# Optimization experiments

Measured on AMD Instinct MI355X. Metric: run time of the kernel, lower is better.

## Reference

```python
import jax, jax.numpy as jnp
import numpy as np

N_SRC = 50000
N_DST = 50000
E = 500000
H = 128
ED = 32
EPS = 1e-5


def _linear_params(key, fan_in, fan_out):
    kw, kb = jax.random.split(key)
    bound = 1.0 / np.sqrt(fan_in)
    W = jax.random.uniform(kw, (fan_in, fan_out), jnp.float32, -bound, bound)
    b = jax.random.uniform(kb, (fan_out,), jnp.float32, -bound, bound)
    return W, b


def setup_inputs() -> dict:
    key = jax.random.key(0)
    ks = jax.random.split(key, 12)
    src_x = jax.random.normal(ks[0], (N_SRC, H), jnp.float32)
    dst_x = jax.random.normal(ks[1], (N_DST, H), jnp.float32)
    edge_index = jax.random.randint(ks[2], (2, E), 0, N_DST, jnp.int64)
    edge_attr = jax.random.normal(ks[3], (E, ED), jnp.float32)
    Wsrc, bsrc = _linear_params(ks[4], H, H)
    Wdst, bdst = _linear_params(ks[5], H, H)
    We, be = _linear_params(ks[6], ED, H)
    Wattn, battn = _linear_params(ks[7], 3 * H, 1)
    Wmsg, bmsg = _linear_params(ks[8], H, H)
    Wout, bout = _linear_params(ks[9], 2 * H, H)
    gamma = jnp.ones((H,), jnp.float32)
    beta = jnp.zeros((H,), jnp.float32)
    return dict(src_x=src_x, dst_x=dst_x, edge_index=edge_index, edge_attr=edge_attr,
                Wsrc=Wsrc, bsrc=bsrc, Wdst=Wdst, bdst=bdst, We=We, be=be,
                Wattn=Wattn, battn=battn, Wmsg=Wmsg, bmsg=bmsg,
                Wout=Wout, bout=bout, gamma=gamma, beta=beta)


def _segment_softmax(scores, idx, num_segments):
    # numerically stable softmax over variable-size segments of dst index
    m = jax.ops.segment_max(scores, idx, num_segments=num_segments)
    ex = jnp.exp(scores - m[idx])
    s = jax.ops.segment_sum(ex, idx, num_segments=num_segments)
    return ex / s[idx]


def reference(src_x, dst_x, edge_index, edge_attr,
              Wsrc, bsrc, Wdst, bdst, We, be,
              Wattn, battn, Wmsg, bmsg, Wout, bout, gamma, beta):
    src_idx = edge_index[0]
    dst_idx = edge_index[1]
    num_dst = dst_x.shape[0]

    src_feat = src_x[src_idx] @ Wsrc + bsrc          # [E, H]
    dst_feat = dst_x[dst_idx] @ Wdst + bdst          # [E, H]
    e_feat = edge_attr @ We + be                     # [E, H]

    attn_in = jnp.concatenate([src_feat, dst_feat, e_feat], axis=-1)  # [E, 3H]
    msg = (src_feat + e_feat) @ Wmsg + bmsg          # [E, H]

    scores = (jnp.tanh(attn_in) @ Wattn + battn)[:, 0]  # [E]
    alpha = _segment_softmax(scores, dst_idx, num_dst)   # [E]

    agg = jax.ops.segment_sum(msg * alpha[:, None], dst_idx, num_segments=num_dst)  # [num_dst, H]

    updated = jnp.concatenate([dst_x, agg], axis=-1) @ Wout + bout
    # dropout is identity in eval mode
    h = dst_x + updated
    mu = jnp.mean(h, axis=-1, keepdims=True)
    var = jnp.var(h, axis=-1, keepdims=True)
    return (h - mu) * jax.lax.rsqrt(var + EPS) * gamma + beta
```

## Files before the change

kernel.cpp:

```cpp
#include <hip/hip_runtime.h>
#include <math.h>

#define NSRC 50000
#define NDST 50000
#define NE   500000
#define HD   128
#define EDIM 32
#define LN_EPS 1e-5f

typedef __attribute__((ext_vector_type(8))) short short8;
typedef __attribute__((ext_vector_type(4))) float f32x4;
typedef unsigned short u16;

#define TL2E 2.8853900817779268f
#define L2E  1.4426950408889634f

__device__ __forceinline__ float EXP2(float x) {
#if __has_builtin(__builtin_amdgcn_exp2f)
    return __builtin_amdgcn_exp2f(x);
#else
    return exp2f(x);
#endif
}
__device__ __forceinline__ float RCP(float x) {
#if __has_builtin(__builtin_amdgcn_rcpf)
    return __builtin_amdgcn_rcpf(x);
#else
    return 1.f / x;
#endif
}
__device__ __forceinline__ u16 f2b(float x) {
    unsigned u = __float_as_uint(x);
    return (u16)((u + 0x7FFFu + ((u >> 16) & 1u)) >> 16);
}
__device__ __forceinline__ float b2f(u16 h) {
    return __uint_as_float(((unsigned)h) << 16);
}
__device__ __forceinline__ short8 ld8(const u16* p) { return *(const short8*)p; }

__global__ __launch_bounds__(128) void fold1_kernel(
    const float* __restrict__ Wsrc, const float* __restrict__ bsrc,
    const float* __restrict__ We,   const float* __restrict__ be,
    const float* __restrict__ Wmsg, const float* __restrict__ bmsg,
    float* __restrict__ Wsm, float* __restrict__ bsm,
    float* __restrict__ WeMsg, float* __restrict__ c2,
    int* __restrict__ cnt)
{
    const int j = threadIdx.x;
    const int r = blockIdx.x;
    if (r >= 162) {
        int i = (r - 162) * 128 + j;
        if (i < NDST + 16) cnt[i] = 0;
        return;
    }
    float s = 0.f;
    if (r < 128) {
        for (int k = 0; k < 128; ++k) s += Wsrc[r*HD + k] * Wmsg[k*HD + j];
        Wsm[r*HD + j] = s;
    } else if (r < 160) {
        const int rr = r - 128;
        for (int k = 0; k < 128; ++k) s += We[rr*HD + k] * Wmsg[k*HD + j];
        WeMsg[rr*HD + j] = s;
    } else if (r == 160) {
        for (int k = 0; k < 128; ++k) s += bsrc[k] * Wmsg[k*HD + j];
        bsm[j] = s + bmsg[j];
    } else {
        for (int k = 0; k < 128; ++k) s += be[k] * Wmsg[k*HD + j];
        c2[j] = s;
    }
}

__global__ __launch_bounds__(64) void pack_all_kernel(
    const float* __restrict__ Wsrc, const float* __restrict__ Wdst,
    const float* __restrict__ Wsm,  const float* __restrict__ Wout,
    const float* __restrict__ We,   const float* __restrict__ WeMsg,
    const float* __restrict__ c2,   const float* __restrict__ bout,
    u16* __restrict__ Wsrc_pk, u16* __restrict__ Wdst_pk,
    u16* __restrict__ Wsm_pk,  u16* __restrict__ W1_pk,
    u16* __restrict__ W2_pk,   u16* __restrict__ We_pk,
    u16* __restrict__ W3_pk,   float* __restrict__ bias2)
{
    const int b = blockIdx.x;
    const int lane = threadIdx.x;
    const int ln = lane & 15, quad = lane >> 4;
    const float* Wout2 = Wout + HD*HD;

    if (b == 176) {
#pragma unroll
        for (int h = 0; h < 2; ++h) {
            const int col = lane + h*64;
            float s = 0.f;
            for (int k = 0; k < 128; ++k) s += c2[k] * Wout2[k*HD + col];
            bias2[col] = bout[col] + s;
        }
        return;
    }
    if (b >= 168) {
        const int t = b - 168;
        const int jj = t*16 + ln;
        float sacc[8] = {0,0,0,0,0,0,0,0};
        for (int k = 0; k < 128; ++k) {
            const float w2 = Wout2[k*HD + jj];
#pragma unroll
            for (int j = 0; j < 8; ++j)
                sacc[j] = fmaf(WeMsg[(quad*8 + j)*HD + k], w2, sacc[j]);
        }
        u16 tmp[8];
#pragma unroll
        for (int j = 0; j < 8; ++j) tmp[j] = f2b(sacc[j]);
        *(short8*)(W3_pk + (size_t)(t*64 + lane)*8) = *(short8*)tmp;
        return;
    }

    const float* src; u16* dst; int lb; float scl = 1.f; bool addI = false;
    if      (b < 32)  { src = Wsrc; dst = Wsrc_pk; lb = b;       scl = TL2E; }
    else if (b < 64)  { src = Wdst; dst = Wdst_pk; lb = b - 32;  scl = TL2E; }
    else if (b < 96)  { src = Wsm;  dst = Wsm_pk;  lb = b - 64; }
    else if (b < 128) { src = Wout; dst = W1_pk;   lb = b - 96;  addI = true; }
    else if (b < 160) { src = Wout2;dst = W2_pk;   lb = b - 128; }
    else              { src = We;   dst = We_pk;   lb = b - 160; scl = TL2E; }
    const int kc = lb >> 3, t = lb & 7;
    u16 tmp[8];
#pragma unroll
    for (int j = 0; j < 8; ++j) {
        const int i = kc*32 + quad*8 + j, jj = t*16 + ln;
        float v = src[(size_t)i*HD + jj] * scl;
        if (addI && i == jj) v += 1.f;
        tmp[j] = f2b(v);
    }
    *(short8*)(dst + (size_t)(lb*64 + lane)*8) = *(short8*)tmp;
}

#define GN 782
#define HB ((NE + 255) / 256)

__global__ __launch_bounds__(256) void mega_kernel(
    const float* __restrict__ src_x, const float* __restrict__ dst_x,
    const int* __restrict__ ei,
    const u16* __restrict__ Wsrc_pk, const u16* __restrict__ Wsm_pk,
    const u16* __restrict__ Wdst_pk,
    const float* __restrict__ bsrc, const float* __restrict__ bsm,
    const float* __restrict__ bdst, const float* __restrict__ wattn,
    float* __restrict__ s1, float* __restrict__ s2,
    u16* __restrict__ srcmsgb, int* __restrict__ cnt, int* __restrict__ rank)
{
    __shared__ u16 lds[4 * 16 * HD];
    const int t = threadIdx.x;
    const int blk = blockIdx.x;

    if (blk >= 2*GN) {
        const int e = (blk - 2*GN) * 256 + t;
        if (e < NE) rank[e] = atomicAdd(&cnt[ei[NE + e]], 1);
        return;
    }

    const int w = t >> 6, lane = t & 63;
    const int ln = lane & 15, quad = lane >> 4;
    const bool is_src = (blk < GN);
    const int b = is_src ? blk : blk - GN;
    int row0 = (b * 4 + w) * 16;
    if (row0 > NSRC - 16) row0 = NSRC - 16;

    const float* xp = (is_src ? src_x : dst_x) + (size_t)(row0 + ln)*HD;
    short8 a[4];
#pragma unroll
    for (int kc = 0; kc < 4; ++kc) {
        float4 f0 = *(const float4*)(xp + kc*32 + quad*8);
        float4 f1 = *(const float4*)(xp + kc*32 + quad*8 + 4);
        u16 tb[8] = { f2b(f0.x), f2b(f0.y), f2b(f0.z), f2b(f0.w),
                      f2b(f1.x), f2b(f1.y), f2b(f1.z), f2b(f1.w) };
        a[kc] = *(short8*)tb;
    }

    const u16*   Wpk = is_src ? Wsrc_pk : Wdst_pk;
    const float* bb_ = is_src ? bsrc : bdst;
    const float* wa  = is_src ? wattn : wattn + HD;
    float* sout      = is_src ? s1 : s2;

    float v[4] = {0.f, 0.f, 0.f, 0.f};
    float ws = 0.f;
#pragma unroll
    for (int tt = 0; tt < 8; ++tt) {
        const float bb = bb_[tt*16 + ln] * TL2E;
        const float ww = wa[tt*16 + ln];
        f32x4 acc = {bb, bb, bb, bb};
#pragma unroll
        for (int kc = 0; kc < 4; ++kc) {
            short8 bfr = ld8(Wpk + (size_t)((kc*8 + tt)*64 + lane)*8);
            acc = __builtin_amdgcn_mfma_f32_16x16x32_bf16(a[kc], bfr, acc, 0, 0, 0);
        }
        ws += ww;
#pragma unroll
        for (int r = 0; r < 4; ++r)
            v[r] = fmaf(ww, RCP(EXP2(acc[r]) + 1.f), v[r]);
    }
#pragma unroll
    for (int off = 8; off >= 1; off >>= 1) {
        ws += __shfl_xor(ws, off);
#pragma unroll
        for (int r = 0; r < 4; ++r) v[r] += __shfl_xor(v[r], off);
    }
    if (ln == 0) {
#pragma unroll
        for (int r = 0; r < 4; ++r)
            sout[row0 + quad*4 + r] = fmaf(-2.f, v[r], ws);
    }

    if (!is_src) return;

#pragma unroll
    for (int tt = 0; tt < 8; ++tt) {
        const float bs = bsm[tt*16 + ln];
        f32x4 acc = {bs, bs, bs, bs};
#pragma unroll
        for (int kc = 0; kc < 4; ++kc) {
            short8 bfr = ld8(Wsm_pk + (size_t)((kc*8 + tt)*64 + lane)*8);
            acc = __builtin_amdgcn_mfma_f32_16x16x32_bf16(a[kc], bfr, acc, 0, 0, 0);
        }
#pragma unroll
        for (int r = 0; r < 4; ++r)
            lds[w*2048 + (quad*4 + r)*HD + tt*16 + ln] = f2b(acc[r]);
    }
    __syncthreads();
#pragma unroll
    for (int r = 0; r < 4; ++r) {
        int idx = r*512 + lane*8;
        short8 val = *(short8*)(lds + w*2048 + idx);
        int row = idx >> 7, col = idx & 127;
        *(short8*)(srcmsgb + (size_t)(row0 + row)*HD + col) = val;
    }
}

__global__ __launch_bounds__(1024) void scan1_kernel(
    const int* __restrict__ cnt, int* __restrict__ excl, int* __restrict__ bsum)
{
    __shared__ int buf[1024];
    const int t = threadIdx.x;
    const int i = blockIdx.x * 1024 + t;
    int v = (i < NDST) ? cnt[i] : 0;
    buf[t] = v;
    __syncthreads();
    for (int off = 1; off < 1024; off <<= 1) {
        int tv = (t >= off) ? buf[t - off] : 0;
        __syncthreads();
        buf[t] += tv;
        __syncthreads();
    }
    if (i < NDST) excl[i] = buf[t] - v;
    if (t == 1023) bsum[blockIdx.x] = buf[1023];
}

__global__ __launch_bounds__(256) void scan23_kernel(
    const int* __restrict__ bsum, int* __restrict__ rowptr)
{
    __shared__ int pref[64];
    const int t = threadIdx.x;
    const int NB = (NDST + 1023) / 1024;
    if (t < 64) {
        int orig = (t < NB) ? bsum[t] : 0;
        int v = orig;
        for (int off = 1; off < 64; off <<= 1) {
            int u = __shfl_up(v, off);
            if (t >= off) v += u;
        }
        pref[t] = v - orig;
        if (blockIdx.x == 0 && t == NB - 1) rowptr[NDST] = v;
    }
    __syncthreads();
    const int i = blockIdx.x * 256 + t;
    if (i < NDST) rowptr[i] += pref[i >> 10];
}

__global__ __launch_bounds__(256) void edge_score_kernel(
    const int* __restrict__ ei, const float* __restrict__ eattr,
    const u16* __restrict__ We_pk, const float* __restrict__ be,
    const float* __restrict__ wattn, const float* __restrict__ battn,
    const float* __restrict__ s1, const float* __restrict__ s2,
    const int* __restrict__ rowptr, const int* __restrict__ rank,
    int4* __restrict__ ev16)
{
    const int t = threadIdx.x;
    const int w = t >> 6, lane = t & 63;
    const int ln = lane & 15, quad = lane >> 4;
    const int e0 = (blockIdx.x * 4 + w) * 16;
    if (e0 >= NE) return;

    const float* ap = eattr + (size_t)(e0 + ln)*EDIM + quad*8;
    float4 f0 = *(const float4*)(ap);
    float4 f1 = *(const float4*)(ap + 4);
    u16 ab[8] = { f2b(f0.x), f2b(f0.y), f2b(f0.z), f2b(f0.w),
                  f2b(f1.x), f2b(f1.y), f2b(f1.z), f2b(f1.w) };
    short8 a = *(short8*)ab;

    const float* wa3 = wattn + 2*HD;
    float v[4] = {0.f, 0.f, 0.f, 0.f};
    float ws = 0.f;
#pragma unroll
    for (int tt = 0; tt < 8; ++tt) {
        const float bb = be[tt*16 + ln] * TL2E;
        const float ww = wa3[tt*16 + ln];
        f32x4 acc = {bb, bb, bb, bb};
        short8 b = ld8(We_pk + (size_t)(tt*64 + lane)*8);
        acc = __builtin_amdgcn_mfma_f32_16x16x32_bf16(a, b, acc, 0, 0, 0);
        ws += ww;
#pragma unroll
        for (int r = 0; r < 4; ++r)
            v[r] = fmaf(ww, RCP(EXP2(acc[r]) + 1.f), v[r]);
    }
#pragma unroll
    for (int off = 8; off >= 1; off >>= 1) {
        ws += __shfl_xor(ws, off);
#pragma unroll
        for (int r = 0; r < 4; ++r) v[r] += __shfl_xor(v[r], off);
    }
    const int srcq = (ln >> 2) << 4;
    float sv0 = __shfl(v[0], srcq);
    float sv1 = __shfl(v[1], srcq);
    float sv2 = __shfl(v[2], srcq);
    float sv3 = __shfl(v[3], srcq);
    const int rr = ln & 3;
    float vlo = (rr & 1) ? sv1 : sv0;
    float vhi = (rr & 1) ? sv3 : sv2;
    float vv  = (rr & 2) ? vhi : vlo;

    if (quad == 0) {
        const int e = e0 + ln;
        const int srcn = ei[e];
        const int dstn = ei[NE + e];
        float sc = (fmaf(-2.f, vv, ws) + s1[srcn] + s2[dstn] + battn[0]) * L2E;
        const int pos = rowptr[dstn] + rank[e];
        ev16[pos] = make_int4(srcn, e, __float_as_int(sc), 0);
    }
}

__global__ __launch_bounds__(256) void dst_agg_kernel(
    const int4* __restrict__ ev16, const int* __restrict__ rowptr,
    const u16* __restrict__ srcmsgb, const float* __restrict__ eattr,
    const float* __restrict__ c2,
    u16* __restrict__ aggSb, u16* __restrict__ weab)
{
    const int lane = threadIdx.x & 63;
    const int d = blockIdx.x * 4 + (threadIdx.x >> 6);
    const int el = lane >> 4, c = lane & 15;
    const int start = rowptr[d], end = rowptr[d + 1];

    if (start == end) {
        if (el == 0) {
            u16 z[8];
#pragma unroll
            for (int j = 0; j < 8; ++j) z[j] = f2b(-c2[c*8 + j]);
            *(short8*)(aggSb + (size_t)d*HD + c*8) = *(short8*)z;
            if (c < 8) {
                u16 zz[4] = {0,0,0,0};
                *(ushort4*)(weab + (size_t)d*EDIM + c*4) = *(ushort4*)zz;
            }
        }
        return;
    }

    float sacc = 0.f;
    float acc[8]  = {0,0,0,0,0,0,0,0};
    float wacc[4] = {0,0,0,0};

    int icur = start + el;
    bool vcur = (icur < end);
    int iicur = vcur ? icur : start;
    int4 q = ev16[iicur];

    for (int i0 = start; i0 < end; i0 += 4) {
        const float wgt = vcur ? EXP2(__int_as_float(q.z)) : 0.f;
        const int   srow = q.x;
        const int   ecur = q.y;
        const int inx = i0 + 4 + el;
        vcur = (inx < end);
        iicur = vcur ? inx : start;
        q = ev16[iicur];

        sacc += wgt;
        short8 sm = ld8(srcmsgb + (size_t)srow*HD + c*8);
#pragma unroll
        for (int j = 0; j < 8; ++j)
            acc[j] = fmaf(wgt, b2f(((u16*)&sm)[j]), acc[j]);
        if (c < 8) {
            float4 f = *(const float4*)(eattr + (size_t)ecur*EDIM + c*4);
            wacc[0] = fmaf(wgt, f.x, wacc[0]);
            wacc[1] = fmaf(wgt, f.y, wacc[1]);
            wacc[2] = fmaf(wgt, f.z, wacc[2]);
            wacc[3] = fmaf(wgt, f.w, wacc[3]);
        }
    }
#pragma unroll
    for (int off = 16; off <= 32; off <<= 1) {
        sacc += __shfl_xor(sacc, off);
#pragma unroll
        for (int j = 0; j < 8; ++j) acc[j] += __shfl_xor(acc[j], off);
#pragma unroll
        for (int j = 0; j < 4; ++j) wacc[j] += __shfl_xor(wacc[j], off);
    }
    const float inv = RCP(sacc);
    if (el == 0) {
        u16 o[8];
#pragma unroll
        for (int j = 0; j < 8; ++j) o[j] = f2b(acc[j] * inv);
        *(short8*)(aggSb + (size_t)d*HD + c*8) = *(short8*)o;
        if (c < 8) {
            u16 o2[4];
#pragma unroll
            for (int j = 0; j < 4; ++j) o2[j] = f2b(wacc[j] * inv);
            *(ushort4*)(weab + (size_t)d*EDIM + c*4) = *(ushort4*)o2;
        }
    }
}

__global__ __launch_bounds__(256) void final_kernel(
    const float* __restrict__ dst_x, const u16* __restrict__ aggSb,
    const u16* __restrict__ weab,
    const u16* __restrict__ W1_pk, const u16* __restrict__ W2_pk,
    const u16* __restrict__ W3_pk, const float* __restrict__ bias2,
    const float* __restrict__ gamma, const float* __restrict__ beta,
    float* __restrict__ out)
{
    const int t = threadIdx.x;
    const int w = t >> 6, lane = t & 63;
    const int ln = lane & 15, quad = lane >> 4;
    int row0 = (blockIdx.x * 4 + w) * 16;
    if (row0 > NDST - 16) row0 = NDST - 16;

    const float* rp = dst_x + (size_t)(row0 + ln)*HD;
    short8 a1[4], a2[4], a3;
#pragma unroll
    for (int kc = 0; kc < 4; ++kc) {
        float4 f0 = *(const float4*)(rp + kc*32 + quad*8);
        float4 f1 = *(const float4*)(rp + kc*32 + quad*8 + 4);
        u16 tb[8] = { f2b(f0.x), f2b(f0.y), f2b(f0.z), f2b(f0.w),
                      f2b(f1.x), f2b(f1.y), f2b(f1.z), f2b(f1.w) };
        a1[kc] = *(short8*)tb;
        a2[kc] = ld8(aggSb + (size_t)(row0 + ln)*HD + kc*32 + quad*8);
    }
    a3 = ld8(weab + (size_t)(row0 + ln)*EDIM + quad*8);

    f32x4 accs[8];
#pragma unroll
    for (int tt = 0; tt < 8; ++tt) {
        const float bb = bias2[tt*16 + ln];
        f32x4 acc = {bb, bb, bb, bb};
#pragma unroll
        for (int kc = 0; kc < 4; ++kc) {
            short8 b = ld8(W1_pk + (size_t)((kc*8 + tt)*64 + lane)*8);
            acc = __builtin_amdgcn_mfma_f32_16x16x32_bf16(a1[kc], b, acc, 0, 0, 0);
        }
#pragma unroll
        for (int kc = 0; kc < 4; ++kc) {
            short8 b = ld8(W2_pk + (size_t)((kc*8 + tt)*64 + lane)*8);
            acc = __builtin_amdgcn_mfma_f32_16x16x32_bf16(a2[kc], b, acc, 0, 0, 0);
        }
        {
            short8 b = ld8(W3_pk + (size_t)(tt*64 + lane)*8);
            acc = __builtin_amdgcn_mfma_f32_16x16x32_bf16(a3, b, acc, 0, 0, 0);
        }
        accs[tt] = acc;
    }

    const float gl[8] = { gamma[ln], gamma[16+ln], gamma[32+ln], gamma[48+ln],
                          gamma[64+ln], gamma[80+ln], gamma[96+ln], gamma[112+ln] };
    const float bl[8] = { beta[ln], beta[16+ln], beta[32+ln], beta[48+ln],
                          beta[64+ln], beta[80+ln], beta[96+ln], beta[112+ln] };
#pragma unroll
    for (int r = 0; r < 4; ++r) {
        float s = 0.f, qq = 0.f;
#pragma unroll
        for (int tt = 0; tt < 8; ++tt) {
            float u = accs[tt][r];
            s += u; qq += u*u;
        }
#pragma unroll
        for (int off = 8; off >= 1; off >>= 1) {
            s  += __shfl_xor(s, off);
            qq += __shfl_xor(qq, off);
        }
        const float mean = s * (1.f / HD);
        const float var  = qq * (1.f / HD) - mean * mean;
        const float rstd = rsqrtf(var + LN_EPS);
        const int row = row0 + quad*4 + r;
#pragma unroll
        for (int tt = 0; tt < 8; ++tt)
            out[(size_t)row*HD + tt*16 + ln] =
                (accs[tt][r] - mean) * rstd * gl[tt] + bl[tt];
    }
}

extern "C" void kernel_launch(void* const* d_in, const int* in_sizes, int n_in,
                              void* d_out, int out_size, void* d_ws, size_t ws_size,
                              hipStream_t stream)
{
    const float* src_x = (const float*)d_in[0];
    const float* dst_x = (const float*)d_in[1];
    const int*   ei    = (const int*)d_in[2];
    const float* eattr = (const float*)d_in[3];
    const float* Wsrc  = (const float*)d_in[4];
    const float* bsrc  = (const float*)d_in[5];
    const float* Wdst  = (const float*)d_in[6];
    const float* bdst  = (const float*)d_in[7];
    const float* We    = (const float*)d_in[8];
    const float* be    = (const float*)d_in[9];
    const float* Wattn = (const float*)d_in[10];
    const float* battn = (const float*)d_in[11];
    const float* Wmsg  = (const float*)d_in[12];
    const float* bmsg  = (const float*)d_in[13];
    const float* Wout  = (const float*)d_in[14];
    const float* bout  = (const float*)d_in[15];
    const float* gamma = (const float*)d_in[16];
    const float* beta  = (const float*)d_in[17];
    float* out = (float*)d_out;

    float* ws = (float*)d_ws;
    u16* srcmsgb = (u16*)(ws + 0);
    u16* aggSb   = (u16*)(ws + 3200000);
    u16* weab    = (u16*)(ws + 6400000);
    float* s1    = ws + 7200000;
    float* s2    = ws + 7250048;
    float* Wsm   = ws + 7300096;
    float* bsm   = ws + 7316480;
    float* WeMsg = ws + 7316608;
    float* c2    = ws + 7320704;
    float* bias2 = ws + 7320832;
    u16* Wsrc_pk = (u16*)(ws + 7320960);
    u16* Wdst_pk = (u16*)(ws + 7329152);
    u16* Wsm_pk  = (u16*)(ws + 7337344);
    u16* W1_pk   = (u16*)(ws + 7345536);
    u16* W2_pk   = (u16*)(ws + 7353728);
    u16* We_pk   = (u16*)(ws + 7361920);
    u16* W3_pk   = (u16*)(ws + 7363968);
    int* rowptr  = (int*)(ws + 7366016);
    int* cnt     = (int*)(ws + 7416032);
    int* bsum    = (int*)(ws + 7466048);
    int* rank    = (int*)(ws + 7466112);
    int4* ev16   = (int4*)(ws + 7966112);

    fold1_kernel<<<553, 128, 0, stream>>>(Wsrc, bsrc, We, be, Wmsg, bmsg,
                                          Wsm, bsm, WeMsg, c2, cnt);
    pack_all_kernel<<<177, 64, 0, stream>>>(Wsrc, Wdst, Wsm, Wout, We, WeMsg,
                                            c2, bout,
                                            Wsrc_pk, Wdst_pk, Wsm_pk, W1_pk,
                                            W2_pk, We_pk, W3_pk, bias2);

    mega_kernel<<<2*GN + HB, 256, 0, stream>>>(
        src_x, dst_x, ei, Wsrc_pk, Wsm_pk, Wdst_pk,
        bsrc, bsm, bdst, Wattn, s1, s2, srcmsgb, cnt, rank);

    scan1_kernel<<<(NDST + 1023) / 1024, 1024, 0, stream>>>(cnt, rowptr, bsum);
    scan23_kernel<<<(NDST + 255) / 256, 256, 0, stream>>>(bsum, rowptr);

    edge_score_kernel<<<(NE/16 + 3) / 4, 256, 0, stream>>>(
        ei, eattr, We_pk, be, Wattn, battn, s1, s2, rowptr, rank, ev16);

    dst_agg_kernel<<<NDST / 4, 256, 0, stream>>>(ev16, rowptr, srcmsgb,
                                                 eattr, c2, aggSb, weab);

    final_kernel<<<GN, 256, 0, stream>>>(dst_x, aggSb, weab, W1_pk, W2_pk, W3_pk,
                                         bias2, gamma, beta, out);
}
```

Measured before the change: 305.8 us.

## Merge weight prep kernels, stage weights in LDS, process 32 rows per wave

Merges the fold and pack preprocessing kernels into one prep kernel that computes Wsrc·Wmsg, We·Wmsg and the folded biases directly in packed bf16 form, removing a launch and the intermediate fp32 buffers. In mega_kernel each wave now handles two 16-row tiles that share B fragments staged once per block in LDS, and the message tile store uses an XOR-swizzled LDS layout. The edge-count atomics are vectorized to four edges per thread. The cost is more LDS and registers per block and extra redundant FMA work in the small prep blocks.

```diff
diff --git a/kernel.cpp b/kernel.cpp
--- a/kernel.cpp
+++ b/kernel.cpp
@@ -38,92 +38,112 @@
 }
 __device__ __forceinline__ short8 ld8(const u16* p) { return *(const short8*)p; }
 
-__global__ __launch_bounds__(128) void fold1_kernel(
+__global__ __launch_bounds__(64) void prep_kernel(
     const float* __restrict__ Wsrc, const float* __restrict__ bsrc,
-    const float* __restrict__ We,   const float* __restrict__ be,
-    const float* __restrict__ Wmsg, const float* __restrict__ bmsg,
-    float* __restrict__ Wsm, float* __restrict__ bsm,
-    float* __restrict__ WeMsg, float* __restrict__ c2,
-    int* __restrict__ cnt)
-{
-    const int j = threadIdx.x;
-    const int r = blockIdx.x;
-    if (r >= 162) {
-        int i = (r - 162) * 128 + j;
-        if (i < NDST + 16) cnt[i] = 0;
-        return;
-    }
-    float s = 0.f;
-    if (r < 128) {
-        for (int k = 0; k < 128; ++k) s += Wsrc[r*HD + k] * Wmsg[k*HD + j];
-        Wsm[r*HD + j] = s;
-    } else if (r < 160) {
-        const int rr = r - 128;
-        for (int k = 0; k < 128; ++k) s += We[rr*HD + k] * Wmsg[k*HD + j];
-        WeMsg[rr*HD + j] = s;
-    } else if (r == 160) {
-        for (int k = 0; k < 128; ++k) s += bsrc[k] * Wmsg[k*HD + j];
-        bsm[j] = s + bmsg[j];
-    } else {
-        for (int k = 0; k < 128; ++k) s += be[k] * Wmsg[k*HD + j];
-        c2[j] = s;
-    }
-}
-
-__global__ __launch_bounds__(64) void pack_all_kernel(
-    const float* __restrict__ Wsrc, const float* __restrict__ Wdst,
-    const float* __restrict__ Wsm,  const float* __restrict__ Wout,
-    const float* __restrict__ We,   const float* __restrict__ WeMsg,
-    const float* __restrict__ c2,   const float* __restrict__ bout,
+    const float* __restrict__ Wdst, const float* __restrict__ We,
+    const float* __restrict__ be,   const float* __restrict__ Wmsg,
+    const float* __restrict__ bmsg, const float* __restrict__ Wout,
+    const float* __restrict__ bout,
     u16* __restrict__ Wsrc_pk, u16* __restrict__ Wdst_pk,
-    u16* __restrict__ Wsm_pk,  u16* __restrict__ W1_pk,
-    u16* __restrict__ W2_pk,   u16* __restrict__ We_pk,
-    u16* __restrict__ W3_pk,   float* __restrict__ bias2)
-{
+    u16* __restrict__ W1_pk,   u16* __restrict__ W2_pk,
+    u16* __restrict__ We_pk,   u16* __restrict__ Wsm_pk,
+    u16* __restrict__ W3_pk,
+    float* __restrict__ bsm, float* __restrict__ c2g,
+    float* __restrict__ bias2, int* __restrict__ cnt)
+{
+    __shared__ float sbuf[32 * 128];
     const int b = blockIdx.x;
     const int lane = threadIdx.x;
+
+    if (b >= 178) {
+        const int i4 = (b - 178) * 64 + lane;
+        if (i4 < 12504) ((int4*)cnt)[i4] = make_int4(0, 0, 0, 0);
+        return;
+    }
+
     const int ln = lane & 15, quad = lane >> 4;
     const float* Wout2 = Wout + HD*HD;
 
+    if (b == 177) {
+#pragma unroll
+        for (int h = 0; h < 2; ++h) {
+            const int col = lane + h*64;
+            float s = bmsg[col];
+            for (int m = 0; m < 128; ++m) s = fmaf(bsrc[m], Wmsg[m*HD + col], s);
+            bsm[col] = s;
+        }
+        return;
+    }
     if (b == 176) {
 #pragma unroll
         for (int h = 0; h < 2; ++h) {
             const int col = lane + h*64;
             float s = 0.f;
-            for (int k = 0; k < 128; ++k) s += c2[k] * Wout2[k*HD + col];
-            bias2[col] = bout[col] + s;
+            for (int m = 0; m < 128; ++m) s = fmaf(be[m], Wmsg[m*HD + col], s);
+            sbuf[col] = s;
+            c2g[col] = s;
+        }
+        __syncthreads();
+#pragma unroll
+        for (int h = 0; h < 2; ++h) {
+            const int col = lane + h*64;
+            float s = bout[col];
+            for (int k = 0; k < 128; ++k) s = fmaf(sbuf[k], Wout2[k*HD + col], s);
+            bias2[col] = s;
         }
         return;
     }
     if (b >= 168) {
-        const int t = b - 168;
-        const int jj = t*16 + ln;
-        float sacc[8] = {0,0,0,0,0,0,0,0};
+        const int tq = b - 168;
+        const int i = lane >> 1, k0 = (lane & 1) * 64;
+        for (int k = k0; k < k0 + 64; ++k) {
+            float s = 0.f;
+            for (int m = 0; m < 128; ++m) s = fmaf(We[i*HD + m], Wmsg[m*HD + k], s);
+            sbuf[i*128 + k] = s;
+        }
+        __syncthreads();
+        const int jj = tq*16 + ln;
+        float s[8] = {0,0,0,0,0,0,0,0};
         for (int k = 0; k < 128; ++k) {
             const float w2 = Wout2[k*HD + jj];
 #pragma unroll
             for (int j = 0; j < 8; ++j)
-                sacc[j] = fmaf(WeMsg[(quad*8 + j)*HD + k], w2, sacc[j]);
+                s[j] = fmaf(sbuf[(quad*8 + j)*128 + k], w2, s[j]);
         }
         u16 tmp[8];
 #pragma unroll
-        for (int j = 0; j < 8; ++j) tmp[j] = f2b(sacc[j]);
-        *(short8*)(W3_pk + (size_t)(t*64 + lane)*8) = *(short8*)tmp;
+        for (int j = 0; j < 8; ++j) tmp[j] = f2b(s[j]);
+        *(short8*)(W3_pk + (size_t)(tq*64 + lane)*8) = *(short8*)tmp;
         return;
     }
+    if (b >= 136) {
+        const int lb = b - 136, kc = lb >> 3, tq = lb & 7;
+        const int jj = tq*16 + ln;
+        float s[8] = {0,0,0,0,0,0,0,0};
+        for (int k = 0; k < 128; ++k) {
+            const float wm = Wmsg[k*HD + jj];
+#pragma unroll
+            for (int j = 0; j < 8; ++j)
+                s[j] = fmaf(Wsrc[(size_t)(kc*32 + quad*8 + j)*HD + k], wm, s[j]);
+        }
+        u16 tmp[8];
+#pragma unroll
+        for (int j = 0; j < 8; ++j) tmp[j] = f2b(s[j]);
+        *(short8*)(Wsm_pk + (size_t)(lb*64 + lane)*8) = *(short8*)tmp;
+        return;
+    }
 
     const float* src; u16* dst; int lb; float scl = 1.f; bool addI = false;
-    if      (b < 32)  { src = Wsrc; dst = Wsrc_pk; lb = b;       scl = TL2E; }
-    else if (b < 64)  { src = Wdst; dst = Wdst_pk; lb = b - 32;  scl = TL2E; }
-    else if (b < 96)  { src = Wsm;  dst = Wsm_pk;  lb = b - 64; }
-    else if (b < 128) { src = Wout; dst = W1_pk;   lb = b - 96;  addI = true; }
-    else if (b < 160) { src = Wout2;dst = W2_pk;   lb = b - 128; }
-    else              { src = We;   dst = We_pk;   lb = b - 160; scl = TL2E; }
-    const int kc = lb >> 3, t = lb & 7;
+    if      (b < 32)  { src = Wsrc;  dst = Wsrc_pk; lb = b;       scl = TL2E; }
+    else if (b < 64)  { src = Wdst;  dst = Wdst_pk; lb = b - 32;  scl = TL2E; }
+    else if (b < 96)  { src = Wout;  dst = W1_pk;   lb = b - 64;  addI = true; }
+    else if (b < 128) { src = Wout2; dst = W2_pk;   lb = b - 96; }
+    else              { src = We;    dst = We_pk;   lb = b - 128; scl = TL2E; }
+    const int kc = lb >> 3, tq = lb & 7;
     u16 tmp[8];
 #pragma unroll
     for (int j = 0; j < 8; ++j) {
-        const int i = kc*32 + quad*8 + j, jj = t*16 + ln;
+        const int i = kc*32 + quad*8 + j, jj = tq*16 + ln;
         float v = src[(size_t)i*HD + jj] * scl;
         if (addI && i == jj) v += 1.f;
         tmp[j] = f2b(v);
@@ -131,8 +151,8 @@
     *(short8*)(dst + (size_t)(lb*64 + lane)*8) = *(short8*)tmp;
 }
 
-#define GN 782
-#define HB ((NE + 255) / 256)
+#define NBLK 391
+#define HB4 ((NE/4 + 255) / 256)
 
 __global__ __launch_bounds__(256) void mega_kernel(
     const float* __restrict__ src_x, const float* __restrict__ dst_x,
@@ -144,90 +164,135 @@
     float* __restrict__ s1, float* __restrict__ s2,
     u16* __restrict__ srcmsgb, int* __restrict__ cnt, int* __restrict__ rank)
 {
-    __shared__ u16 lds[4 * 16 * HD];
+    __shared__ __align__(16) u16 wlds[16384];
+    __shared__ __align__(16) u16 tlds[4][2048];
     const int t = threadIdx.x;
     const int blk = blockIdx.x;
 
-    if (blk >= 2*GN) {
-        const int e = (blk - 2*GN) * 256 + t;
-        if (e < NE) rank[e] = atomicAdd(&cnt[ei[NE + e]], 1);
+    if (blk >= 2*NBLK) {
+        const int idx = (blk - 2*NBLK) * 256 + t;
+        if (idx < NE/4) {
+            int4 d4 = ((const int4*)(ei + NE))[idx];
+            int4 r4;
+            r4.x = atomicAdd(&cnt[d4.x], 1);
+            r4.y = atomicAdd(&cnt[d4.y], 1);
+            r4.z = atomicAdd(&cnt[d4.z], 1);
+            r4.w = atomicAdd(&cnt[d4.w], 1);
+            ((int4*)rank)[idx] = r4;
+        }
         return;
     }
 
     const int w = t >> 6, lane = t & 63;
     const int ln = lane & 15, quad = lane >> 4;
-    const bool is_src = (blk < GN);
-    const int b = is_src ? blk : blk - GN;
-    int row0 = (b * 4 + w) * 16;
-    if (row0 > NSRC - 16) row0 = NSRC - 16;
-
-    const float* xp = (is_src ? src_x : dst_x) + (size_t)(row0 + ln)*HD;
-    short8 a[4];
+    const bool is_src = (blk < NBLK);
+    const int b = is_src ? blk : blk - NBLK;
+    int row0 = b * 128 + w * 32;
+    if (row0 > NSRC - 32) row0 = NSRC - 32;
+
+    const float* X = is_src ? src_x : dst_x;
+    const float* rp0 = X + (size_t)(row0 + ln)*HD;
+    const float* rp1 = rp0 + (size_t)16*HD;
+    short8 a0[4], a1[4];
 #pragma unroll
     for (int kc = 0; kc < 4; ++kc) {
-        float4 f0 = *(const float4*)(xp + kc*32 + quad*8);
-        float4 f1 = *(const float4*)(xp + kc*32 + quad*8 + 4);
+        float4 f0 = *(const float4*)(rp0 + kc*32 + quad*8);
+        float4 f1 = *(const float4*)(rp0 + kc*32 + quad*8 + 4);
+        float4 g0 = *(const float4*)(rp1 + kc*32 + quad*8);
+        float4 g1 = *(const float4*)(rp1 + kc*32 + quad*8 + 4);
         u16 tb[8] = { f2b(f0.x), f2b(f0.y), f2b(f0.z), f2b(f0.w),
                       f2b(f1.x), f2b(f1.y), f2b(f1.z), f2b(f1.w) };
-        a[kc] = *(short8*)tb;
-    }
-
-    const u16*   Wpk = is_src ? Wsrc_pk : Wdst_pk;
+        a0[kc] = *(short8*)tb;
+        u16 tc[8] = { f2b(g0.x), f2b(g0.y), f2b(g0.z), f2b(g0.w),
+                      f2b(g1.x), f2b(g1.y), f2b(g1.z), f2b(g1.w) };
+        a1[kc] = *(short8*)tc;
+    }
+
+    const u16* Wpk = is_src ? Wsrc_pk : Wdst_pk;
+#pragma unroll
+    for (int it = 0; it < 8; ++it) {
+        short8 v = ld8(Wpk + (size_t)(it*256 + t)*8);
+        *(short8*)(&wlds[(it*256 + t)*8]) = v;
+    }
+    __syncthreads();
+
     const float* bb_ = is_src ? bsrc : bdst;
     const float* wa  = is_src ? wattn : wattn + HD;
     float* sout      = is_src ? s1 : s2;
 
-    float v[4] = {0.f, 0.f, 0.f, 0.f};
+    float v0[4] = {0,0,0,0}, v1[4] = {0,0,0,0};
     float ws = 0.f;
 #pragma unroll
     for (int tt = 0; tt < 8; ++tt) {
         const float bb = bb_[tt*16 + ln] * TL2E;
         const float ww = wa[tt*16 + ln];
-        f32x4 acc = {bb, bb, bb, bb};
+        f32x4 acc0 = {bb, bb, bb, bb};
+        f32x4 acc1 = {bb, bb, bb, bb};
 #pragma unroll
         for (int kc = 0; kc < 4; ++kc) {
-            short8 bfr = ld8(Wpk + (size_t)((kc*8 + tt)*64 + lane)*8);
-            acc = __builtin_amdgcn_mfma_f32_16x16x32_bf16(a[kc], bfr, acc, 0, 0, 0);
+            short8 bf = ld8(&wlds[(size_t)((kc*8 + tt)*64 + lane)*8]);
+            acc0 = __builtin_amdgcn_mfma_f32_16x16x32_bf16(a0[kc], bf, acc0, 0, 0, 0);
+            acc1 = __builtin_amdgcn_mfma_f32_16x16x32_bf16(a1[kc], bf, acc1, 0, 0, 0);
         }
         ws += ww;
 #pragma unroll
-        for (int r = 0; r < 4; ++r)
-            v[r] = fmaf(ww, RCP(EXP2(acc[r]) + 1.f), v[r]);
+        for (int r = 0; r < 4; ++r) {
+            v0[r] = fmaf(ww, RCP(EXP2(acc0[r]) + 1.f), v0[r]);
+            v1[r] = fmaf(ww, RCP(EXP2(acc1[r]) + 1.f), v1[r]);
+        }
     }
 #pragma unroll
     for (int off = 8; off >= 1; off >>= 1) {
         ws += __shfl_xor(ws, off);
 #pragma unroll
-        for (int r = 0; r < 4; ++r) v[r] += __shfl_xor(v[r], off);
+        for (int r = 0; r < 4; ++r) {
+            v0[r] += __shfl_xor(v0[r], off);
+            v1[r] += __shfl_xor(v1[r], off);
+        }
     }
     if (ln == 0) {
 #pragma unroll
-        for (int r = 0; r < 4; ++r)
-            sout[row0 + quad*4 + r] = fmaf(-2.f, v[r], ws);
+        for (int r = 0; r < 4; ++r) {
+            sout[row0 + quad*4 + r]      = fmaf(-2.f, v0[r], ws);
+            sout[row0 + 16 + quad*4 + r] = fmaf(-2.f, v1[r], ws);
+        }
     }
 
     if (!is_src) return;
 
-#pragma unroll
-    for (int tt = 0; tt < 8; ++tt) {
-        const float bs = bsm[tt*16 + ln];
-        f32x4 acc = {bs, bs, bs, bs};
-#pragma unroll
-        for (int kc = 0; kc < 4; ++kc) {
-            short8 bfr = ld8(Wsm_pk + (size_t)((kc*8 + tt)*64 + lane)*8);
-            acc = __builtin_amdgcn_mfma_f32_16x16x32_bf16(a[kc], bfr, acc, 0, 0, 0);
-        }
-#pragma unroll
-        for (int r = 0; r < 4; ++r)
-            lds[w*2048 + (quad*4 + r)*HD + tt*16 + ln] = f2b(acc[r]);
-    }
     __syncthreads();
 #pragma unroll
-    for (int r = 0; r < 4; ++r) {
-        int idx = r*512 + lane*8;
-        short8 val = *(short8*)(lds + w*2048 + idx);
-        int row = idx >> 7, col = idx & 127;
-        *(short8*)(srcmsgb + (size_t)(row0 + row)*HD + col) = val;
+    for (int it = 0; it < 8; ++it) {
+        short8 v = ld8(Wsm_pk + (size_t)(it*256 + t)*8);
+        *(short8*)(&wlds[(it*256 + t)*8]) = v;
+    }
+    __syncthreads();
+
+    u16* slab = &tlds[w][0];
+#pragma unroll
+    for (int tile = 0; tile < 2; ++tile) {
+#pragma unroll
+        for (int tt = 0; tt < 8; ++tt) {
+            const float bs = bsm[tt*16 + ln];
+            f32x4 acc = {bs, bs, bs, bs};
+#pragma unroll
+            for (int kc = 0; kc < 4; ++kc) {
+                short8 bf = ld8(&wlds[(size_t)((kc*8 + tt)*64 + lane)*8]);
+                acc = __builtin_amdgcn_mfma_f32_16x16x32_bf16(
+                          tile ? a1[kc] : a0[kc], bf, acc, 0, 0, 0);
+            }
+#pragma unroll
+            for (int r = 0; r < 4; ++r)
+                slab[(quad*4 + r)*128 + ((tt ^ quad) << 4) + ln] = f2b(acc[r]);
+        }
+#pragma unroll
+        for (int r2 = 0; r2 < 4; ++r2) {
+            const int row = r2*4 + quad;
+            const int c = ln*8;
+            const int sidx = row*128 + (((c >> 4) ^ r2) << 4) + (c & 15);
+            short8 val = *(const short8*)(&slab[sidx]);
+            *(short8*)(srcmsgb + (size_t)(row0 + tile*16 + row)*HD + c) = val;
+        }
     }
 }
 
@@ -519,32 +584,28 @@
     u16* weab    = (u16*)(ws + 6400000);
     float* s1    = ws + 7200000;
     float* s2    = ws + 7250048;
-    float* Wsm   = ws + 7300096;
-    float* bsm   = ws + 7316480;
-    float* WeMsg = ws + 7316608;
-    float* c2    = ws + 7320704;
-    float* bias2 = ws + 7320832;
-    u16* Wsrc_pk = (u16*)(ws + 7320960);
-    u16* Wdst_pk = (u16*)(ws + 7329152);
-    u16* Wsm_pk  = (u16*)(ws + 7337344);
-    u16* W1_pk   = (u16*)(ws + 7345536);
-    u16* W2_pk   = (u16*)(ws + 7353728);
-    u16* We_pk   = (u16*)(ws + 7361920);
-    u16* W3_pk   = (u16*)(ws + 7363968);
-    int* rowptr  = (int*)(ws + 7366016);
-    int* cnt     = (int*)(ws + 7416032);
-    int* bsum    = (int*)(ws + 7466048);
-    int* rank    = (int*)(ws + 7466112);
-    int4* ev16   = (int4*)(ws + 7966112);
-
-    fold1_kernel<<<553, 128, 0, stream>>>(Wsrc, bsrc, We, be, Wmsg, bmsg,
-                                          Wsm, bsm, WeMsg, c2, cnt);
-    pack_all_kernel<<<177, 64, 0, stream>>>(Wsrc, Wdst, Wsm, Wout, We, WeMsg,
-                                            c2, bout,
-                                            Wsrc_pk, Wdst_pk, Wsm_pk, W1_pk,
-                                            W2_pk, We_pk, W3_pk, bias2);
-
-    mega_kernel<<<2*GN + HB, 256, 0, stream>>>(
+    float* bsm   = ws + 7300096;
+    float* c2    = ws + 7300224;
+    float* bias2 = ws + 7300352;
+    u16* Wsrc_pk = (u16*)(ws + 7300480);
+    u16* Wdst_pk = (u16*)(ws + 7308672);
+    u16* Wsm_pk  = (u16*)(ws + 7316864);
+    u16* W1_pk   = (u16*)(ws + 7325056);
+    u16* W2_pk   = (u16*)(ws + 7333248);
+    u16* We_pk   = (u16*)(ws + 7341440);
+    u16* W3_pk   = (u16*)(ws + 7343488);
+    int* rowptr  = (int*)(ws + 7345536);
+    int* cnt     = (int*)(ws + 7395552);
+    int* bsum    = (int*)(ws + 7445568);
+    int* rank    = (int*)(ws + 7445632);
+    int4* ev16   = (int4*)(ws + 7945632);
+
+    prep_kernel<<<374, 64, 0, stream>>>(Wsrc, bsrc, Wdst, We, be, Wmsg, bmsg,
+                                        Wout, bout,
+                                        Wsrc_pk, Wdst_pk, W1_pk, W2_pk, We_pk,
+                                        Wsm_pk, W3_pk, bsm, c2, bias2, cnt);
+
+    mega_kernel<<<2*NBLK + HB4, 256, 0, stream>>>(
         src_x, dst_x, ei, Wsrc_pk, Wsm_pk, Wdst_pk,
         bsrc, bsm, bdst, Wattn, s1, s2, srcmsgb, cnt, rank);
 
@@ -557,6 +618,6 @@
     dst_agg_kernel<<<NDST / 4, 256, 0, stream>>>(ev16, rowptr, srcmsgb,
                                                  eattr, c2, aggSb, weab);
 
-    final_kernel<<<GN, 256, 0, stream>>>(dst_x, aggSb, weab, W1_pk, W2_pk, W3_pk,
-                                         bias2, gamma, beta, out);
-}
+    final_kernel<<<(NDST/16 + 3) / 4, 256, 0, stream>>>(
+        dst_x, aggSb, weab, W1_pk, W2_pk, W3_pk, bias2, gamma, beta, out);
+}
```

Result: slower. 492.9 us (+61.2%).

## Stage weights in LDS, process two row tiles per wave, vectorize degree count

Applied to the files above, without the earlier changes.

The node-projection part of mega_kernel now copies each packed 128x128 weight matrix into LDS once per block. Each wave handles 32 rows as two 16-row MFMA tiles that share the same B fragments, which halves the block count and cuts repeated global weight loads. The srcmsg staging buffer gains an XOR swizzle to avoid LDS bank conflicts. The edge-count atomics now read four dst indices per thread as an int4 and write ranks as an int4. The trade-offs are more LDS and register use per block, which may lower occupancy, plus extra barriers for the weight reloads.

```diff
diff --git a/kernel.cpp b/kernel.cpp
--- a/kernel.cpp
+++ b/kernel.cpp
@@ -131,8 +131,8 @@
     *(short8*)(dst + (size_t)(lb*64 + lane)*8) = *(short8*)tmp;
 }
 
-#define GN 782
-#define HB ((NE + 255) / 256)
+#define NBLK 391
+#define HB4 ((NE/4 + 255) / 256)
 
 __global__ __launch_bounds__(256) void mega_kernel(
     const float* __restrict__ src_x, const float* __restrict__ dst_x,
@@ -144,90 +144,135 @@
     float* __restrict__ s1, float* __restrict__ s2,
     u16* __restrict__ srcmsgb, int* __restrict__ cnt, int* __restrict__ rank)
 {
-    __shared__ u16 lds[4 * 16 * HD];
+    __shared__ __align__(16) u16 wlds[16384];
+    __shared__ __align__(16) u16 tlds[4][2048];
     const int t = threadIdx.x;
     const int blk = blockIdx.x;
 
-    if (blk >= 2*GN) {
-        const int e = (blk - 2*GN) * 256 + t;
-        if (e < NE) rank[e] = atomicAdd(&cnt[ei[NE + e]], 1);
+    if (blk >= 2*NBLK) {
+        const int idx = (blk - 2*NBLK) * 256 + t;
+        if (idx < NE/4) {
+            int4 d4 = ((const int4*)(ei + NE))[idx];
+            int4 r4;
+            r4.x = atomicAdd(&cnt[d4.x], 1);
+            r4.y = atomicAdd(&cnt[d4.y], 1);
+            r4.z = atomicAdd(&cnt[d4.z], 1);
+            r4.w = atomicAdd(&cnt[d4.w], 1);
+            ((int4*)rank)[idx] = r4;
+        }
         return;
     }
 
     const int w = t >> 6, lane = t & 63;
     const int ln = lane & 15, quad = lane >> 4;
-    const bool is_src = (blk < GN);
-    const int b = is_src ? blk : blk - GN;
-    int row0 = (b * 4 + w) * 16;
-    if (row0 > NSRC - 16) row0 = NSRC - 16;
-
-    const float* xp = (is_src ? src_x : dst_x) + (size_t)(row0 + ln)*HD;
-    short8 a[4];
+    const bool is_src = (blk < NBLK);
+    const int b = is_src ? blk : blk - NBLK;
+    int row0 = b * 128 + w * 32;
+    if (row0 > NSRC - 32) row0 = NSRC - 32;
+
+    const float* X = is_src ? src_x : dst_x;
+    const float* rp0 = X + (size_t)(row0 + ln)*HD;
+    const float* rp1 = rp0 + (size_t)16*HD;
+    short8 a0[4], a1[4];
 #pragma unroll
     for (int kc = 0; kc < 4; ++kc) {
-        float4 f0 = *(const float4*)(xp + kc*32 + quad*8);
-        float4 f1 = *(const float4*)(xp + kc*32 + quad*8 + 4);
+        float4 f0 = *(const float4*)(rp0 + kc*32 + quad*8);
+        float4 f1 = *(const float4*)(rp0 + kc*32 + quad*8 + 4);
+        float4 g0 = *(const float4*)(rp1 + kc*32 + quad*8);
+        float4 g1 = *(const float4*)(rp1 + kc*32 + quad*8 + 4);
         u16 tb[8] = { f2b(f0.x), f2b(f0.y), f2b(f0.z), f2b(f0.w),
                       f2b(f1.x), f2b(f1.y), f2b(f1.z), f2b(f1.w) };
-        a[kc] = *(short8*)tb;
-    }
-
-    const u16*   Wpk = is_src ? Wsrc_pk : Wdst_pk;
+        a0[kc] = *(short8*)tb;
+        u16 tc[8] = { f2b(g0.x), f2b(g0.y), f2b(g0.z), f2b(g0.w),
+                      f2b(g1.x), f2b(g1.y), f2b(g1.z), f2b(g1.w) };
+        a1[kc] = *(short8*)tc;
+    }
+
+    const u16* Wpk = is_src ? Wsrc_pk : Wdst_pk;
+#pragma unroll
+    for (int it = 0; it < 8; ++it) {
+        short8 v = ld8(Wpk + (size_t)(it*256 + t)*8);
+        *(short8*)(&wlds[(it*256 + t)*8]) = v;
+    }
+    __syncthreads();
+
     const float* bb_ = is_src ? bsrc : bdst;
     const float* wa  = is_src ? wattn : wattn + HD;
     float* sout      = is_src ? s1 : s2;
 
-    float v[4] = {0.f, 0.f, 0.f, 0.f};
+    float v0[4] = {0,0,0,0}, v1[4] = {0,0,0,0};
     float ws = 0.f;
 #pragma unroll
     for (int tt = 0; tt < 8; ++tt) {
         const float bb = bb_[tt*16 + ln] * TL2E;
         const float ww = wa[tt*16 + ln];
-        f32x4 acc = {bb, bb, bb, bb};
+        f32x4 acc0 = {bb, bb, bb, bb};
+        f32x4 acc1 = {bb, bb, bb, bb};
 #pragma unroll
         for (int kc = 0; kc < 4; ++kc) {
-            short8 bfr = ld8(Wpk + (size_t)((kc*8 + tt)*64 + lane)*8);
-            acc = __builtin_amdgcn_mfma_f32_16x16x32_bf16(a[kc], bfr, acc, 0, 0, 0);
+            short8 bf = ld8(&wlds[(size_t)((kc*8 + tt)*64 + lane)*8]);
+            acc0 = __builtin_amdgcn_mfma_f32_16x16x32_bf16(a0[kc], bf, acc0, 0, 0, 0);
+            acc1 = __builtin_amdgcn_mfma_f32_16x16x32_bf16(a1[kc], bf, acc1, 0, 0, 0);
         }
         ws += ww;
 #pragma unroll
-        for (int r = 0; r < 4; ++r)
-            v[r] = fmaf(ww, RCP(EXP2(acc[r]) + 1.f), v[r]);
+        for (int r = 0; r < 4; ++r) {
+            v0[r] = fmaf(ww, RCP(EXP2(acc0[r]) + 1.f), v0[r]);
+            v1[r] = fmaf(ww, RCP(EXP2(acc1[r]) + 1.f), v1[r]);
+        }
     }
 #pragma unroll
     for (int off = 8; off >= 1; off >>= 1) {
         ws += __shfl_xor(ws, off);
 #pragma unroll
-        for (int r = 0; r < 4; ++r) v[r] += __shfl_xor(v[r], off);
+        for (int r = 0; r < 4; ++r) {
+            v0[r] += __shfl_xor(v0[r], off);
+            v1[r] += __shfl_xor(v1[r], off);
+        }
     }
     if (ln == 0) {
 #pragma unroll
-        for (int r = 0; r < 4; ++r)
-            sout[row0 + quad*4 + r] = fmaf(-2.f, v[r], ws);
+        for (int r = 0; r < 4; ++r) {
+            sout[row0 + quad*4 + r]      = fmaf(-2.f, v0[r], ws);
+            sout[row0 + 16 + quad*4 + r] = fmaf(-2.f, v1[r], ws);
+        }
     }
 
     if (!is_src) return;
 
-#pragma unroll
-    for (int tt = 0; tt < 8; ++tt) {
-        const float bs = bsm[tt*16 + ln];
-        f32x4 acc = {bs, bs, bs, bs};
-#pragma unroll
-        for (int kc = 0; kc < 4; ++kc) {
-            short8 bfr = ld8(Wsm_pk + (size_t)((kc*8 + tt)*64 + lane)*8);
-            acc = __builtin_amdgcn_mfma_f32_16x16x32_bf16(a[kc], bfr, acc, 0, 0, 0);
-        }
-#pragma unroll
-        for (int r = 0; r < 4; ++r)
-            lds[w*2048 + (quad*4 + r)*HD + tt*16 + ln] = f2b(acc[r]);
-    }
     __syncthreads();
 #pragma unroll
-    for (int r = 0; r < 4; ++r) {
-        int idx = r*512 + lane*8;
-        short8 val = *(short8*)(lds + w*2048 + idx);
-        int row = idx >> 7, col = idx & 127;
-        *(short8*)(srcmsgb + (size_t)(row0 + row)*HD + col) = val;
+    for (int it = 0; it < 8; ++it) {
+        short8 v = ld8(Wsm_pk + (size_t)(it*256 + t)*8);
+        *(short8*)(&wlds[(it*256 + t)*8]) = v;
+    }
+    __syncthreads();
+
+    u16* slab = &tlds[w][0];
+#pragma unroll
+    for (int tile = 0; tile < 2; ++tile) {
+#pragma unroll
+        for (int tt = 0; tt < 8; ++tt) {
+            const float bs = bsm[tt*16 + ln];
+            f32x4 acc = {bs, bs, bs, bs};
+#pragma unroll
+            for (int kc = 0; kc < 4; ++kc) {
+                short8 bf = ld8(&wlds[(size_t)((kc*8 + tt)*64 + lane)*8]);
+                acc = __builtin_amdgcn_mfma_f32_16x16x32_bf16(
+                          tile ? a1[kc] : a0[kc], bf, acc, 0, 0, 0);
+            }
+#pragma unroll
+            for (int r = 0; r < 4; ++r)
+                slab[(quad*4 + r)*128 + ((tt ^ quad) << 4) + ln] = f2b(acc[r]);
+        }
+#pragma unroll
+        for (int r2 = 0; r2 < 4; ++r2) {
+            const int row = r2*4 + quad;
+            const int c = ln*8;
+            const int sidx = row*128 + (((c >> 4) ^ r2) << 4) + (c & 15);
+            short8 val = *(const short8*)(&slab[sidx]);
+            *(short8*)(srcmsgb + (size_t)(row0 + tile*16 + row)*HD + c) = val;
+        }
     }
 }
 
@@ -544,7 +589,7 @@
                                             Wsrc_pk, Wdst_pk, Wsm_pk, W1_pk,
                                             W2_pk, We_pk, W3_pk, bias2);
 
-    mega_kernel<<<2*GN + HB, 256, 0, stream>>>(
+    mega_kernel<<<2*NBLK + HB4, 256, 0, stream>>>(
         src_x, dst_x, ei, Wsrc_pk, Wsm_pk, Wdst_pk,
         bsrc, bsm, bdst, Wattn, s1, s2, srcmsgb, cnt, rank);
 
@@ -557,6 +602,6 @@
     dst_agg_kernel<<<NDST / 4, 256, 0, stream>>>(ev16, rowptr, srcmsgb,
                                                  eattr, c2, aggSb, weab);
 
-    final_kernel<<<GN, 256, 0, stream>>>(dst_x, aggSb, weab, W1_pk, W2_pk, W3_pk,
-                                         bias2, gamma, beta, out);
-}
+    final_kernel<<<(NDST/16 + 3) / 4, 256, 0, stream>>>(
+        dst_x, aggSb, weab, W1_pk, W2_pk, W3_pk, bias2, gamma, beta, out);
+}
```

Measured after the change: 303.2 us. No clear change (-0.9%).
